# Kernel tuning notes

Hardware: AMD Instinct MI355X
Metric: run time of the kernel (lower is better)

Reference implementation:

```python
import jax, jax.numpy as jnp
import numpy as np

B, L, G, N, K, E = 64, 512, 128, 32, 8, 65536
NTOK, D_TOK, H_DIR, NTL_INP, NHID, NREL = 10000, 64, 64, 32, 16, 16


def _bn(x, gamma, beta, eps=1e-5):
    # training-mode BatchNorm1d over axis 0; x: (n, C)
    mu = x.mean(0)
    var = x.var(0)
    return gamma * (x - mu) / jnp.sqrt(var + eps) + beta


def _lstm(x, w_ih, w_hh, b_ih, b_hh):
    # x: (B, T, D); torch gate order i, f, g, o
    nb = x.shape[0]
    H = w_hh.shape[1]
    def step(carry, xt):
        h, c = carry
        g = xt @ w_ih.T + b_ih + h @ w_hh.T + b_hh
        i, f, gg, o = jnp.split(g, 4, axis=-1)
        c = jax.nn.sigmoid(f) * c + jax.nn.sigmoid(i) * jnp.tanh(gg)
        h = jax.nn.sigmoid(o) * jnp.tanh(c)
        return (h, c), h
    init = (jnp.zeros((nb, H), x.dtype), jnp.zeros((nb, H), x.dtype))
    _, hs = jax.lax.scan(step, init, jnp.swapaxes(x, 0, 1))
    return jnp.swapaxes(hs, 0, 1)


def setup_inputs() -> dict:
    key = jax.random.key(0)
    ks = jax.random.split(key, 24)
    inp = {}
    inp['seq'] = jax.random.randint(ks[0], (B, L), 0, NTOK)
    inp['pos2grp'] = jax.random.randint(ks[1], (B, L), 0, G)
    inp['idx'] = jax.random.randint(ks[2], (B, N, K), 0, L)
    inp['u'] = jax.random.randint(ks[3], (E,), 0, B * N)
    inp['v'] = jax.random.randint(ks[4], (E,), 0, B * N)
    # parameters
    s = 1.0 / np.sqrt(H_DIR)
    inp['tok_emb'] = jax.random.normal(ks[5], (NTOK, D_TOK), jnp.float32)
    for tag, k0 in (('f', 6), ('b', 10)):
        inp[f'w_ih_{tag}'] = s * jax.random.normal(ks[k0], (4 * H_DIR, D_TOK), jnp.float32)
        inp[f'w_hh_{tag}'] = s * jax.random.normal(ks[k0 + 1], (4 * H_DIR, H_DIR), jnp.float32)
        inp[f'b_ih_{tag}'] = s * jax.random.normal(ks[k0 + 2], (4 * H_DIR,), jnp.float32)
        inp[f'b_hh_{tag}'] = s * jax.random.normal(ks[k0 + 3], (4 * H_DIR,), jnp.float32)
    inp['w_src'] = (1.0 / np.sqrt(2 * H_DIR)) * jax.random.normal(ks[14], (NTL_INP, 2 * H_DIR), jnp.float32)
    inp['b_src'] = jnp.zeros((NTL_INP,), jnp.float32)
    inp['w_dst'] = (1.0 / np.sqrt(2 * H_DIR)) * jax.random.normal(ks[15], (NTL_INP, 2 * H_DIR), jnp.float32)
    inp['b_dst'] = jnp.zeros((NTL_INP,), jnp.float32)
    inp['g_src'] = jnp.ones((NTL_INP,), jnp.float32)
    inp['be_src'] = jnp.zeros((NTL_INP,), jnp.float32)
    inp['g_dst'] = jnp.ones((NTL_INP,), jnp.float32)
    inp['be_dst'] = jnp.zeros((NTL_INP,), jnp.float32)
    inp['ntl_w'] = 0.001 * jax.random.normal(ks[16], (NREL, NHID, NTL_INP, NTL_INP), jnp.float32)
    inp['ntl_v'] = 0.001 * jax.random.normal(ks[17], (NREL, NHID, 2 * NTL_INP), jnp.float32)
    inp['ntl_b'] = jnp.zeros((NREL, NHID, 1), jnp.float32)
    inp['ntl_u'] = 0.001 * jax.random.normal(ks[18], (NREL, 1, NHID), jnp.float32)
    inp['ntl_g'] = jnp.ones((NREL * NHID,), jnp.float32)
    inp['ntl_be'] = jnp.zeros((NREL * NHID,), jnp.float32)
    return inp


def reference(seq, pos2grp, idx, u, v, tok_emb,
              w_ih_f, w_hh_f, b_ih_f, b_hh_f,
              w_ih_b, w_hh_b, b_ih_b, b_hh_b,
              w_src, b_src, w_dst, b_dst,
              g_src, be_src, g_dst, be_dst,
              ntl_w, ntl_v, ntl_b, ntl_u, ntl_g, ntl_be):
    # token embed + scatter-sum tokens -> groups
    x_tok = tok_emb[seq]                                   # (B, L, D)
    gid = (pos2grp + jnp.arange(B)[:, None] * G).reshape(-1)
    x_grp = jax.ops.segment_sum(x_tok.reshape(B * L, -1), gid,
                                num_segments=B * G).reshape(B, G, -1)
    # bidirectional LSTM over groups
    hf = _lstm(x_grp, w_ih_f, w_hh_f, b_ih_f, b_hh_f)
    hb = jnp.flip(_lstm(jnp.flip(x_grp, 1), w_ih_b, w_hh_b, b_ih_b, b_hh_b), 1)
    h_grp = jnp.concatenate([hf, hb], -1)                  # (B, G, 2H)
    # hierarchical gather + sum: node <- sum over K token positions' groups
    b_idx = jnp.arange(B)[:, None, None]
    g_idx = pos2grp[b_idx, idx]                            # (B, N, K)
    h = h_grp[b_idx, g_idx].sum(2).reshape(B * N, -1)      # (B*N, 2H)
    # edge endpoint projections + batchnorm
    hs = _bn(h[u] @ w_src.T + b_src, g_src, be_src)        # (E, ninp)
    ht = _bn(h[v] @ w_dst.T + b_dst, g_dst, be_dst)
    # Neural Tensor Layer
    linear = jnp.einsum('rhd,nd->rhn', ntl_v, jnp.concatenate([hs, ht], 1))
    bil = jnp.stack([
        jnp.einsum('nhj,nj->hn', jnp.einsum('ni,hij->nhj', hs, ntl_w[r]), ht)
        for r in range(NREL)], 0)                          # (R, H, E)
    z = bil + linear + ntl_b
    mu = z.mean(-1, keepdims=True)
    var = z.var(-1, keepdims=True)
    zn = ntl_g.reshape(NREL, NHID, 1) * (z - mu) / jnp.sqrt(var + 1e-5) \
         + ntl_be.reshape(NREL, NHID, 1)
    t = jnp.tanh(zn)
    logit = jnp.einsum('rh,rhn->nr', ntl_u[:, 0, :], t)    # (E, R)
    return logit
```

## Files before the change

kernel.cpp:

```cpp
#include <hip/hip_runtime.h>
#include <hip/hip_bf16.h>
#include <hip/hip_fp16.h>
#include <cstdint>

constexpr int B_   = 64;
constexpr int L_   = 512;
constexpr int G_   = 128;
constexpr int E_   = 65536;
constexpr int RH   = 256;
constexpr int M_   = 2048;
constexpr int JA   = 33;
constexpr int COLS = RH * JA;
constexpr int NREP = 16;

typedef _Float16 v2h __attribute__((ext_vector_type(2)));
typedef _Float16 v8h __attribute__((ext_vector_type(8)));
typedef float    v4f __attribute__((ext_vector_type(4)));
typedef float    v2f32 __attribute__((ext_vector_type(2)));
typedef union { uint4 u4; v8h h8; } cvt8;

#define DEV static __device__ __forceinline__

DEV float sigm(float x) { return 1.f / (1.f + __expf(-x)); }
DEV float tanh_fast(float x) {
    x = fminf(15.f, fmaxf(-15.f, x));
    float e = __expf(2.f * x);
    return (e - 1.f) / (e + 1.f);
}

__global__ __launch_bounds__(256) void k_eh(const int* __restrict__ seq,
                                            const int* __restrict__ p2g,
                                            const float* __restrict__ emb,
                                            const int* __restrict__ u,
                                            const int* __restrict__ v,
                                            const float* __restrict__ ntlw,
                                            const float* __restrict__ ntlv,
                                            const float* __restrict__ ntlb,
                                            float* __restrict__ xg,
                                            int* __restrict__ cu, int* __restrict__ cv,
                                            float* __restrict__ waug) {
    int blk = blockIdx.x;
    int t   = threadIdx.x;
    if (blk >= 512) {
        int gid = (blk - 512) * 256 + t;
        int i   = gid / COLS;
        int rem = gid - i * COLS;
        int rh  = rem / JA;
        int j   = rem - rh * JA;
        float val;
        if (i < 32) val = (j < 32) ? ntlw[((size_t)rh * 32 + i) * 32 + j] : ntlv[rh * 64 + i];
        else        val = (j < 32) ? ntlv[rh * 64 + 32 + j] : ntlb[rh];
        waug[(size_t)i * COLS + j * 256 + rh] = val;
        return;
    }
    if (blk >= 256) {
        int n = (blk - 256) * 256 + t;
        atomicAdd(&cu[u[n]], 1);
        atomicAdd(&cv[v[n]], 1);
        return;
    }
    __shared__ float xgl[G_ * 64];
    __shared__ int sl[128], gld[128];
    int b = blk >> 2, part = blk & 3;
    for (int i = t; i < G_ * 64; i += 256) xgl[i] = 0.f;
    if (t < 128) {
        sl[t]  = seq[b * L_ + part * 128 + t];
        gld[t] = p2g[b * L_ + part * 128 + t];
    }
    __syncthreads();
    int d = t & 63, sub = t >> 6;
#pragma unroll
    for (int gg = 0; gg < 2; gg++) {
        int sv[16], gv[16];
#pragma unroll
        for (int k = 0; k < 16; k++) {
            sv[k] = sl[sub * 32 + gg * 16 + k];
            gv[k] = gld[sub * 32 + gg * 16 + k];
        }
#pragma unroll
        for (int k = 0; k < 16; k++)
            atomicAdd(&xgl[gv[k] * 64 + d], emb[(size_t)sv[k] * 64 + d]);
    }
    __syncthreads();
    for (int i = t; i < G_ * 64; i += 256)
        atomicAdd(&xg[(size_t)b * G_ * 64 + i], xgl[i]);
}

__global__ __launch_bounds__(256) void k_pre(const float* __restrict__ xg,
                                             const float* __restrict__ wihf,
                                             const float* __restrict__ bihf,
                                             const float* __restrict__ bhhf,
                                             const float* __restrict__ wihb,
                                             const float* __restrict__ bihb,
                                             const float* __restrict__ bhhb,
                                             float* __restrict__ pre,
                                             const int* __restrict__ cu,
                                             int* __restrict__ ustart,
                                             int* __restrict__ ucursor) {
    int blk = blockIdx.x;
    int t   = threadIdx.x;
    if (blk == 512) {
        __shared__ int ps[256];
        int base = t * 8, run = 0;
        int c[8], loc[8];
#pragma unroll
        for (int i = 0; i < 8; i++) c[i] = cu[base + i];
#pragma unroll
        for (int i = 0; i < 8; i++) { loc[i] = run; run += c[i]; }
        ps[t] = run;
        __syncthreads();
        for (int off = 1; off < 256; off <<= 1) {
            int a = (t >= off) ? ps[t - off] : 0;
            __syncthreads();
            ps[t] += a;
            __syncthreads();
        }
        int ex = ps[t] - run;
#pragma unroll
        for (int i = 0; i < 8; i++) { ustart[base + i] = ex + loc[i]; ucursor[base + i] = ex + loc[i]; }
        if (t == 255) ustart[2048] = E_;
        return;
    }
    int dir = blk >> 8;
    const float* wih = dir ? wihb : wihf;
    float bias = dir ? (bihb[t] + bhhb[t]) : (bihf[t] + bhhf[t]);
    int r0 = (blk & 255) * 32;

    float4 wv[16];
#pragma unroll
    for (int c = 0; c < 16; c++) wv[c] = ((const float4*)(wih + t * 64))[c];

#pragma unroll 2
    for (int ml = 0; ml < 32; ml++) {
        const float* xr = xg + (size_t)(r0 + ml) * 64;
        float acc = bias;
#pragma unroll
        for (int c = 0; c < 16; c++) {
            float x0 = xr[4 * c], x1 = xr[4 * c + 1], x2 = xr[4 * c + 2], x3 = xr[4 * c + 3];
            acc += x0 * wv[c].x + x1 * wv[c].y + x2 * wv[c].z + x3 * wv[c].w;
        }
        pre[((size_t)dir * 8192 + r0 + ml) * 256 + t] = acc;
    }
}

__global__ __launch_bounds__(128, 1) void k_lstm(const float* __restrict__ pre,
                                                 const float* __restrict__ whh_f,
                                                 const float* __restrict__ whh_b,
                                                 float* __restrict__ hgrp,
                                                 const int* __restrict__ u,
                                                 const int* __restrict__ v,
                                                 int* __restrict__ ucursor,
                                                 int2* __restrict__ eonv) {
    int blk = blockIdx.x;
    int t   = threadIdx.x;
    if (blk >= 128) {
        int n = (blk - 128) * 128 + t;
        int pos = atomicAdd(&ucursor[u[n]], 1);
        eonv[pos] = make_int2(n, v[n]);
        return;
    }
    __shared__ float2 xbuf[2][2][64];
    int wv = t >> 6;
    int e  = t & 63;
    int dir = blk >> 6;
    int b   = blk & 63;
    const float* whh     = dir ? whh_b : whh_f;
    const float* prebase = pre + ((size_t)dir * 8192 + (size_t)b * G_) * 256;
    float* hout = hgrp + (size_t)b * G_ * 128 + dir * 64 + e;

    v2f32 w[64];
    {
        const float4* pa = (const float4*)(whh + (size_t)((2 * wv + 0) * 64 + e) * 64);
        const float4* pb = (const float4*)(whh + (size_t)((2 * wv + 1) * 64 + e) * 64);
#pragma unroll
        for (int c = 0; c < 16; c++) {
            float4 a = pa[c], bb = pb[c];
            w[4 * c + 0] = (v2f32){a.x, bb.x};
            w[4 * c + 1] = (v2f32){a.y, bb.y};
            w[4 * c + 2] = (v2f32){a.z, bb.z};
            w[4 * c + 3] = (v2f32){a.w, bb.w};
        }
    }
    int c0 = wv * 128 + e;
    int c1 = wv * 128 + 64 + e;

    float h = 0.f, creg = 0.f;

    int s0i = dir ? (G_ - 1) : 0;
    int s1i = dir ? (G_ - 2) : 1;
    float q0 = prebase[(size_t)s0i * 256 + c0];
    float q1 = prebase[(size_t)s0i * 256 + c1];
    float r0 = prebase[(size_t)s1i * 256 + c0];
    float r1 = prebase[(size_t)s1i * 256 + c1];

#pragma unroll 1
    for (int step = 0; step < G_; step++) {
        int s  = dir ? (G_ - 1 - step) : step;
        int t2 = (step + 2 < G_) ? step + 2 : G_ - 1;
        int s2 = dir ? (G_ - 1 - t2) : t2;
        const float* pn = prebase + (size_t)s2 * 256;
        float n0 = pn[c0], n1 = pn[c1];

        v2f32 acc[4];
        acc[0] = (v2f32){q0, q1};
        acc[1] = (v2f32){0.f, 0.f};
        acc[2] = (v2f32){0.f, 0.f};
        acc[3] = (v2f32){0.f, 0.f};
#pragma unroll
        for (int j = 0; j < 64; j++) {
            float hv = __int_as_float(__builtin_amdgcn_readlane(__float_as_int(h), j));
            v2f32 hv2 = {hv, hv};
            acc[j & 3] += w[j] * hv2;
        }
        v2f32 sg = (acc[0] + acc[1]) + (acc[2] + acc[3]);

        float ga = wv ? tanh_fast(sg.x) : sigm(sg.x);
        float gb = sigm(sg.y);

        xbuf[step & 1][wv][e] = make_float2(ga, gb);
        __syncthreads();
        float2 oth = xbuf[step & 1][1 - wv][e];

        float ai = wv ? oth.x : ga;
        float af = wv ? oth.y : gb;
        float ag = wv ? ga : oth.x;
        float ao = wv ? gb : oth.y;
        creg = af * creg + ai * ag;
        h    = ao * tanh_fast(creg);
        if (wv == 0) hout[(size_t)s * 128] = h;

        q0 = r0; q1 = r1;
        r0 = n0; r1 = n1;
    }
}

__global__ __launch_bounds__(256) void k_gp(const int* __restrict__ idx,
                                            const int* __restrict__ p2g,
                                            const float* __restrict__ hgrp,
                                            const int* __restrict__ cu,
                                            const int* __restrict__ cv,
                                            const float* __restrict__ wsrc,
                                            const float* __restrict__ bsrc,
                                            const float* __restrict__ wdst,
                                            const float* __restrict__ bdst,
                                            float* __restrict__ Ps, float* __restrict__ Pd,
                                            float* __restrict__ bn_raw) {
    __shared__ __align__(16) float hsl[8][128];
    __shared__ float red[256];
    int m0 = blockIdx.x * 8;
    int t  = threadIdx.x;
    int d = t & 127, mh = t >> 7;
#pragma unroll
    for (int rep = 0; rep < 4; rep++) {
        int ml = rep * 2 + mh;
        int m  = m0 + ml;
        int b  = m >> 5;
        float acc = 0.f;
#pragma unroll
        for (int k = 0; k < 8; k++) {
            int l = idx[m * 8 + k];
            int g = p2g[b * L_ + l];
            acc += hgrp[((size_t)b * G_ + g) * 128 + d];
        }
        hsl[ml][d] = acc;
    }
    __syncthreads();
    int ml = t >> 5, o = t & 31;
    int m  = m0 + ml;
    const float4* hp = (const float4*)&hsl[ml][0];
    float cw_u = (float)cu[m], cw_v = (float)cv[m];
#pragma unroll 1
    for (int side = 0; side < 2; side++) {
        const float* W = side ? wdst : wsrc;
        float4 wr[32];
#pragma unroll
        for (int c = 0; c < 32; c++) wr[c] = ((const float4*)(W + (size_t)o * 128))[c];
        float acc = side ? bdst[o] : bsrc[o];
#pragma unroll
        for (int c = 0; c < 32; c++) {
            float4 h4 = hp[c];
            acc += h4.x * wr[c].x + h4.y * wr[c].y + h4.z * wr[c].z + h4.w * wr[c].w;
        }
        (side ? Pd : Ps)[(size_t)m * 32 + o] = acc;
        float cw = side ? cw_v : cw_u;
        red[t] = cw * acc;
        __syncthreads();
        if (t < 32) {
            float s = 0.f;
#pragma unroll
            for (int i = 0; i < 8; i++) s += red[i * 32 + t];
            atomicAdd(&bn_raw[side * 64 + t], s);
        }
        __syncthreads();
        red[t] = cw * acc * acc;
        __syncthreads();
        if (t < 32) {
            float s = 0.f;
#pragma unroll
            for (int i = 0; i < 8; i++) s += red[i * 32 + t];
            atomicAdd(&bn_raw[side * 64 + 32 + t], s);
        }
        __syncthreads();
    }
}

__global__ __launch_bounds__(256) void k_prep(const float* __restrict__ Ps,
                                              const float* __restrict__ Pd,
                                              const float* __restrict__ bn_raw,
                                              const float* __restrict__ gs,
                                              const float* __restrict__ bes,
                                              const float* __restrict__ gd,
                                              const float* __restrict__ bed,
                                              float* __restrict__ hsaugT,
                                              v2h* __restrict__ htp) {
    int blk = blockIdx.x;
    int t   = threadIdx.x;
    constexpr float invE = 1.f / (float)E_;
    if (blk < 264) {
        int gid = blk * 256 + t;
        int c = gid >> 11;
        int m = gid & 2047;
        float val = 1.f;
        if (c < 32) {
            float mu  = bn_raw[c] * invE;
            float isd = rsqrtf(bn_raw[32 + c] * invE - mu * mu + 1e-5f);
            val = gs[c] * (Ps[(size_t)m * 32 + c] - mu) * isd + bes[c];
        }
        hsaugT[(size_t)c * 2048 + m] = val;
        return;
    }
    int gid = (blk - 264) * 256 + t;
    int m  = gid >> 4;
    int jp = gid & 15;
    int j0 = 2 * jp, j1 = 2 * jp + 1;
    float mu0  = bn_raw[64 + j0] * invE;
    float isd0 = rsqrtf(bn_raw[96 + j0] * invE - mu0 * mu0 + 1e-5f);
    float mu1  = bn_raw[64 + j1] * invE;
    float isd1 = rsqrtf(bn_raw[96 + j1] * invE - mu1 * mu1 + 1e-5f);
    float h0 = gd[j0] * (Pd[(size_t)m * 32 + j0] - mu0) * isd0 + bed[j0];
    float h1 = gd[j1] * (Pd[(size_t)m * 32 + j1] - mu1) * isd1 + bed[j1];
    v2h p;
    p.x = (_Float16)h0; p.y = (_Float16)h1;
    htp[gid] = p;
}

__global__ __launch_bounds__(256, 1) void k_agemm(const float* __restrict__ hsaugT,
                                                  const float* __restrict__ waug,
                                                  v2h* __restrict__ Ah,
                                                  float* __restrict__ A32) {
    int ms = blockIdx.x;
    int jp = blockIdx.y;
    int t  = threadIdx.x;
    int mbase = ms * 128;
    if (jp < 16) {
        float w0[JA], w1[JA];
#pragma unroll
        for (int i = 0; i < JA; i++) {
            w0[i] = waug[(size_t)i * COLS + (2 * jp) * 256 + t];
            w1[i] = waug[(size_t)i * COLS + (2 * jp + 1) * 256 + t];
        }
#pragma unroll 1
        for (int ch = 0; ch < 16; ch++) {
            int m0 = mbase + ch * 8;
            float acc0[8], acc1[8];
#pragma unroll
            for (int ml = 0; ml < 8; ml++) { acc0[ml] = 0.f; acc1[ml] = 0.f; }
#pragma unroll
            for (int i = 0; i < JA; i++) {
                const float* hr = hsaugT + (size_t)i * 2048 + m0;
#pragma unroll
                for (int ml = 0; ml < 8; ml++) {
                    float hv = hr[ml];
                    acc0[ml] += hv * w0[i];
                    acc1[ml] += hv * w1[i];
                }
            }
#pragma unroll
            for (int ml = 0; ml < 8; ml++) {
                v2h p;
                p.x = (_Float16)acc0[ml]; p.y = (_Float16)acc1[ml];
                Ah[(size_t)(m0 + ml) * 4096 + jp * 256 + t] = p;
            }
        }
    } else {
        float w2[JA];
#pragma unroll
        for (int i = 0; i < JA; i++) w2[i] = waug[(size_t)i * COLS + 32 * 256 + t];
#pragma unroll 1
        for (int ch = 0; ch < 16; ch++) {
            int m0 = mbase + ch * 8;
            float acc[8];
#pragma unroll
            for (int ml = 0; ml < 8; ml++) acc[ml] = 0.f;
#pragma unroll
            for (int i = 0; i < JA; i++) {
                const float* hr = hsaugT + (size_t)i * 2048 + m0;
#pragma unroll
                for (int ml = 0; ml < 8; ml++) acc[ml] += hr[ml] * w2[i];
            }
#pragma unroll
            for (int ml = 0; ml < 8; ml++)
                A32[(size_t)(m0 + ml) * 256 + t] = acc[ml];
        }
    }
}

__global__ __launch_bounds__(256) void k_z(const unsigned int* __restrict__ Ah,
                                           const float* __restrict__ A32,
                                           const uint4* __restrict__ htp4,
                                           const int* __restrict__ ustart,
                                           const int2* __restrict__ eonv,
                                           _Float16* __restrict__ zh,
                                           float* __restrict__ zsumR,
                                           float* __restrict__ zsqR) {
    int t    = threadIdx.x;
    int lane = t & 63;
    int uu   = blockIdx.x * 4 + (t >> 6);
    int l15  = lane & 15, quad = lane >> 4;

    uint4 bf[16];
#pragma unroll
    for (int nt = 0; nt < 16; nt++) {
        const unsigned int* bp = Ah + (size_t)uu * 4096 + (quad * 4) * 256 + nt * 16 + l15;
        bf[nt].x = bp[0]; bf[nt].y = bp[256]; bf[nt].z = bp[512]; bf[nt].w = bp[768];
    }
    float a32[16];
#pragma unroll
    for (int nt = 0; nt < 16; nt++) a32[nt] = A32[(size_t)uu * 256 + nt * 16 + l15];

    float s1[16], s2[16];
#pragma unroll
    for (int nt = 0; nt < 16; nt++) { s1[nt] = 0.f; s2[nt] = 0.f; }

    int e0 = ustart[uu], e1 = ustart[uu + 1];
    for (int base = e0; base < e1; base += 16) {
        int ei = min(base + l15, e1 - 1);
        int2 q = eonv[ei];
        uint4 afu = htp4[(size_t)q.y * 4 + quad];
        cvt8 ac; ac.u4 = afu;
        int nrow[4], valid[4];
#pragma unroll
        for (int r = 0; r < 4; r++) {
            int er = quad * 4 + r;
            nrow[r]  = __builtin_amdgcn_ds_bpermute(er << 2, q.x);
            valid[r] = (base + er) < e1;
        }
#pragma unroll
        for (int nt = 0; nt < 16; nt++) {
            cvt8 bc; bc.u4 = bf[nt];
            v4f acc = { a32[nt], a32[nt], a32[nt], a32[nt] };
            acc = __builtin_amdgcn_mfma_f32_16x16x32_f16(ac.h8, bc.h8, acc, 0, 0, 0);
#pragma unroll
            for (int r = 0; r < 4; r++) {
                if (valid[r]) {
                    float z = acc[r];
                    zh[(size_t)nrow[r] * 256 + nt * 16 + l15] = (_Float16)z;
                    s1[nt] += z; s2[nt] += z * z;
                }
            }
        }
    }
    int rep = (blockIdx.x & (NREP - 1)) * 256;
#pragma unroll
    for (int nt = 0; nt < 16; nt++) {
        float a = s1[nt], b = s2[nt];
        a += __shfl_xor(a, 16); a += __shfl_xor(a, 32);
        b += __shfl_xor(b, 16); b += __shfl_xor(b, 32);
        if (quad == 0) {
            atomicAdd(&zsumR[rep + nt * 16 + l15], a);
            atomicAdd(&zsqR[rep + nt * 16 + l15], b);
        }
    }
}

__global__ __launch_bounds__(256) void k_logit(const _Float16* __restrict__ zh,
                                               const float* __restrict__ zsumR,
                                               const float* __restrict__ zsqR,
                                               const float* __restrict__ ntlu,
                                               const float* __restrict__ ntlg,
                                               const float* __restrict__ ntlbe,
                                               float* __restrict__ out) {
    int t  = threadIdx.x;
    int n0 = blockIdx.x * 16;
    float su = 0.f, sq = 0.f;
#pragma unroll
    for (int r = 0; r < NREP; r++) {
        su += zsumR[r * 256 + t];
        sq += zsqR[r * 256 + t];
    }
    float mu  = su / (float)E_;
    float var = sq / (float)E_ - mu * mu;
    float isd = rsqrtf(var + 1e-5f);
    float g   = ntlg[t],  be  = ntlbe[t];
    float uw  = ntlu[t];
    float zv[16];
#pragma unroll
    for (int nl = 0; nl < 16; nl++)
        zv[nl] = (float)zh[(size_t)(n0 + nl) * 256 + t];
#pragma unroll 1
    for (int nl = 0; nl < 16; nl++) {
        float zn  = g * (zv[nl] - mu) * isd + be;
        float val = uw * tanh_fast(zn);
        val += __shfl_xor(val, 1);
        val += __shfl_xor(val, 2);
        val += __shfl_xor(val, 4);
        val += __shfl_xor(val, 8);
        if ((t & 15) == 0) out[(size_t)(n0 + nl) * 16 + (t >> 4)] = val;
    }
}

extern "C" void kernel_launch(void* const* d_in, const int* in_sizes, int n_in,
                              void* d_out, int out_size, void* d_ws, size_t ws_size,
                              hipStream_t stream) {
    const int*   seq   = (const int*)d_in[0];
    const int*   p2g   = (const int*)d_in[1];
    const int*   idx   = (const int*)d_in[2];
    const int*   u     = (const int*)d_in[3];
    const int*   v     = (const int*)d_in[4];
    const float* emb   = (const float*)d_in[5];
    const float* wihf  = (const float*)d_in[6];
    const float* whhf  = (const float*)d_in[7];
    const float* bihf  = (const float*)d_in[8];
    const float* bhhf  = (const float*)d_in[9];
    const float* wihb  = (const float*)d_in[10];
    const float* whhb  = (const float*)d_in[11];
    const float* bihb  = (const float*)d_in[12];
    const float* bhhb  = (const float*)d_in[13];
    const float* wsrc  = (const float*)d_in[14];
    const float* bsrc  = (const float*)d_in[15];
    const float* wdst  = (const float*)d_in[16];
    const float* bdst  = (const float*)d_in[17];
    const float* gs    = (const float*)d_in[18];
    const float* bes   = (const float*)d_in[19];
    const float* gd    = (const float*)d_in[20];
    const float* bed   = (const float*)d_in[21];
    const float* ntlw  = (const float*)d_in[22];
    const float* ntlv  = (const float*)d_in[23];
    const float* ntlb  = (const float*)d_in[24];
    const float* ntlu  = (const float*)d_in[25];
    const float* ntlg  = (const float*)d_in[26];
    const float* ntlbe = (const float*)d_in[27];
    float* out = (float*)d_out;

    char* ws = (char*)d_ws;
    size_t off = 0;
    auto take = [&](size_t bytes) -> char* {
        char* p = ws + off;
        off = (off + bytes + 255) & ~(size_t)255;
        return p;
    };
    int*   cnt_u  = (int*)  take(2048 * 4);
    int*   cnt_v  = (int*)  take(2048 * 4);
    float* zsumR  = (float*)take((size_t)NREP * 256 * 4);
    float* zsqR   = (float*)take((size_t)NREP * 256 * 4);
    float* bn_raw = (float*)take(128 * 4);
    float* x_grp  = (float*)take((size_t)B_ * G_ * 64 * 4);
    size_t zero_bytes = off;
    int*   ucursor = (int*)  take(2048 * 4);
    int*   ustart  = (int*)  take(2049 * 4);
    int2*  eonv    = (int2*) take((size_t)E_ * 8);
    float* pre     = (float*)take((size_t)2 * 8192 * 256 * 4);
    float* hgrp    = (float*)take((size_t)B_ * G_ * 128 * 4);
    float* Psrc    = (float*)take((size_t)M_ * 32 * 4);
    float* Pdst    = (float*)take((size_t)M_ * 32 * 4);
    float* hsaugT  = (float*)take((size_t)36 * 2048 * 4);
    v2h*   htp     = (v2h*)  take((size_t)M_ * 16 * 4);
    float* waug    = (float*)take((size_t)JA * COLS * 4);
    v2h*   Ah      = (v2h*)  take((size_t)M_ * 4096 * 4);
    float* A32     = (float*)take((size_t)M_ * 256 * 4);
    _Float16* zbuf = (_Float16*)take((size_t)E_ * 256 * 2);
    (void)ws_size; (void)in_sizes; (void)n_in; (void)out_size;

    hipMemsetAsync(d_ws, 0, zero_bytes, stream);

    k_eh<<<512 + 1089, 256, 0, stream>>>(seq, p2g, emb, u, v, ntlw, ntlv, ntlb,
                                         x_grp, cnt_u, cnt_v, waug);
    k_pre<<<513, 256, 0, stream>>>(x_grp, wihf, bihf, bhhf, wihb, bihb, bhhb, pre,
                                   cnt_u, ustart, ucursor);
    k_lstm<<<128 + E_ / 128, 128, 0, stream>>>(pre, whhf, whhb, hgrp, u, v, ucursor, eonv);
    k_gp<<<M_ / 8, 256, 0, stream>>>(idx, p2g, hgrp, cnt_u, cnt_v,
                                     wsrc, bsrc, wdst, bdst, Psrc, Pdst, bn_raw);
    k_prep<<<392, 256, 0, stream>>>(Psrc, Pdst, bn_raw, gs, bes, gd, bed, hsaugT, htp);
    k_agemm<<<dim3(16, 17), 256, 0, stream>>>(hsaugT, waug, Ah, A32);
    k_z<<<512, 256, 0, stream>>>((const unsigned int*)Ah, A32, (const uint4*)htp,
                                 ustart, eonv, zbuf, zsumR, zsqR);
    k_logit<<<E_ / 16, 256, 0, stream>>>(zbuf, zsumR, zsqR, ntlu, ntlg, ntlbe, out);
}
```

Baseline: 387.7 us.

## Split LSTM recurrence across 256 threads, one gate row per thread

The recurrent LSTM kernel now gives each of 256 threads one gate row instead of 128 threads holding two rows each, which halves the per-thread weight registers and the serial dot-product length. Gates are gathered across lanes with shuffles, and the new hidden state is shared through a small LDS buffer, one barrier per step. The edge-bucketing side blocks now use 256 threads, so the grid shrinks to keep the same total work. The cost is more LDS traffic and cross-lane shuffles on the per-step critical path.

```diff
diff --git a/kernel.cpp b/kernel.cpp
--- a/kernel.cpp
+++ b/kernel.cpp
@@ -16,7 +16,6 @@
 typedef _Float16 v2h __attribute__((ext_vector_type(2)));
 typedef _Float16 v8h __attribute__((ext_vector_type(8)));
 typedef float    v4f __attribute__((ext_vector_type(4)));
-typedef float    v2f32 __attribute__((ext_vector_type(2)));
 typedef union { uint4 u4; v8h h8; } cvt8;
 
 #define DEV static __device__ __forceinline__
@@ -143,7 +142,7 @@
     }
 }
 
-__global__ __launch_bounds__(128, 1) void k_lstm(const float* __restrict__ pre,
+__global__ __launch_bounds__(256, 1) void k_lstm(const float* __restrict__ pre,
                                                  const float* __restrict__ whh_f,
                                                  const float* __restrict__ whh_b,
                                                  float* __restrict__ hgrp,
@@ -154,83 +153,72 @@
     int blk = blockIdx.x;
     int t   = threadIdx.x;
     if (blk >= 128) {
-        int n = (blk - 128) * 128 + t;
+        int n = (blk - 128) * 256 + t;
         int pos = atomicAdd(&ucursor[u[n]], 1);
         eonv[pos] = make_int2(n, v[n]);
         return;
     }
-    __shared__ float2 xbuf[2][2][64];
-    int wv = t >> 6;
-    int e  = t & 63;
-    int dir = blk >> 6;
-    int b   = blk & 63;
+    __shared__ float hx[2][64];
+    int l    = t & 63;
+    int q    = t >> 6;
+    int gate = l >> 4;
+    int k    = l & 15;
+    int unit = q * 16 + k;
+    int r    = gate * 64 + unit;
+    int dir  = blk >> 6;
+    int b    = blk & 63;
     const float* whh     = dir ? whh_b : whh_f;
     const float* prebase = pre + ((size_t)dir * 8192 + (size_t)b * G_) * 256;
-    float* hout = hgrp + (size_t)b * G_ * 128 + dir * 64 + e;
-
-    v2f32 w[64];
-    {
-        const float4* pa = (const float4*)(whh + (size_t)((2 * wv + 0) * 64 + e) * 64);
-        const float4* pb = (const float4*)(whh + (size_t)((2 * wv + 1) * 64 + e) * 64);
-#pragma unroll
-        for (int c = 0; c < 16; c++) {
-            float4 a = pa[c], bb = pb[c];
-            w[4 * c + 0] = (v2f32){a.x, bb.x};
-            w[4 * c + 1] = (v2f32){a.y, bb.y};
-            w[4 * c + 2] = (v2f32){a.z, bb.z};
-            w[4 * c + 3] = (v2f32){a.w, bb.w};
-        }
-    }
-    int c0 = wv * 128 + e;
-    int c1 = wv * 128 + 64 + e;
-
-    float h = 0.f, creg = 0.f;
+
+    float4 wv[16];
+#pragma unroll
+    for (int c = 0; c < 16; c++) wv[c] = ((const float4*)(whh + (size_t)r * 64))[c];
+
+    float hreg = 0.f;
+    float creg = 0.f;
 
     int s0i = dir ? (G_ - 1) : 0;
     int s1i = dir ? (G_ - 2) : 1;
-    float q0 = prebase[(size_t)s0i * 256 + c0];
-    float q1 = prebase[(size_t)s0i * 256 + c1];
-    float r0 = prebase[(size_t)s1i * 256 + c0];
-    float r1 = prebase[(size_t)s1i * 256 + c1];
+    float pq = prebase[(size_t)s0i * 256 + r];
+    float pr = prebase[(size_t)s1i * 256 + r];
 
 #pragma unroll 1
     for (int step = 0; step < G_; step++) {
         int s  = dir ? (G_ - 1 - step) : step;
         int t2 = (step + 2 < G_) ? step + 2 : G_ - 1;
         int s2 = dir ? (G_ - 1 - t2) : t2;
-        const float* pn = prebase + (size_t)s2 * 256;
-        float n0 = pn[c0], n1 = pn[c1];
-
-        v2f32 acc[4];
-        acc[0] = (v2f32){q0, q1};
-        acc[1] = (v2f32){0.f, 0.f};
-        acc[2] = (v2f32){0.f, 0.f};
-        acc[3] = (v2f32){0.f, 0.f};
-#pragma unroll
-        for (int j = 0; j < 64; j++) {
-            float hv = __int_as_float(__builtin_amdgcn_readlane(__float_as_int(h), j));
-            v2f32 hv2 = {hv, hv};
-            acc[j & 3] += w[j] * hv2;
-        }
-        v2f32 sg = (acc[0] + acc[1]) + (acc[2] + acc[3]);
-
-        float ga = wv ? tanh_fast(sg.x) : sigm(sg.x);
-        float gb = sigm(sg.y);
-
-        xbuf[step & 1][wv][e] = make_float2(ga, gb);
+        float pn = prebase[(size_t)s2 * 256 + r];
+
+        float a0 = pq, a1 = 0.f, a2 = 0.f, a3 = 0.f;
+#pragma unroll
+        for (int c = 0; c < 16; c++) {
+            float h0 = __int_as_float(__builtin_amdgcn_readlane(__float_as_int(hreg), 4 * c + 0));
+            float h1 = __int_as_float(__builtin_amdgcn_readlane(__float_as_int(hreg), 4 * c + 1));
+            float h2 = __int_as_float(__builtin_amdgcn_readlane(__float_as_int(hreg), 4 * c + 2));
+            float h3 = __int_as_float(__builtin_amdgcn_readlane(__float_as_int(hreg), 4 * c + 3));
+            a0 += wv[c].x * h0;
+            a1 += wv[c].y * h1;
+            a2 += wv[c].z * h2;
+            a3 += wv[c].w * h3;
+        }
+        float gpre = (a0 + a1) + (a2 + a3);
+        float gval = (gate == 2) ? tanh_fast(gpre) : sigm(gpre);
+
+        float gi = __shfl(gval, k);
+        float gf = __shfl(gval, 16 + k);
+        float gg = __shfl(gval, 32 + k);
+        float go = __shfl(gval, 48 + k);
+        creg = gf * creg + gi * gg;
+        float hnew = go * tanh_fast(creg);
+
+        if (gate == 0) {
+            hgrp[((size_t)(b * G_ + s)) * 128 + dir * 64 + unit] = hnew;
+            hx[step & 1][unit] = hnew;
+        }
         __syncthreads();
-        float2 oth = xbuf[step & 1][1 - wv][e];
-
-        float ai = wv ? oth.x : ga;
-        float af = wv ? oth.y : gb;
-        float ag = wv ? ga : oth.x;
-        float ao = wv ? gb : oth.y;
-        creg = af * creg + ai * ag;
-        h    = ao * tanh_fast(creg);
-        if (wv == 0) hout[(size_t)s * 128] = h;
-
-        q0 = r0; q1 = r1;
-        r0 = n0; r1 = n1;
+        hreg = hx[step & 1][l];
+
+        pq = pr; pr = pn;
     }
 }
 
@@ -577,7 +565,7 @@
                                          x_grp, cnt_u, cnt_v, waug);
     k_pre<<<513, 256, 0, stream>>>(x_grp, wihf, bihf, bhhf, wihb, bihb, bhhb, pre,
                                    cnt_u, ustart, ucursor);
-    k_lstm<<<128 + E_ / 128, 128, 0, stream>>>(pre, whhf, whhb, hgrp, u, v, ucursor, eonv);
+    k_lstm<<<384, 256, 0, stream>>>(pre, whhf, whhb, hgrp, u, v, ucursor, eonv);
     k_gp<<<M_ / 8, 256, 0, stream>>>(idx, p2g, hgrp, cnt_u, cnt_v,
                                      wsrc, bsrc, wdst, bdst, Psrc, Pdst, bn_raw);
     k_prep<<<392, 256, 0, stream>>>(Psrc, Pdst, bn_raw, gs, bes, gd, bed, hsaugT, htp);
```

New measurement: 366.5 us. 5.5% less time.
